# Kernel tuning notes

Measured on AMD Instinct MI355X. Metric: run time of the kernel, lower is better.

The kernel has to match this reference:

```python
import jax, jax.numpy as jnp
import numpy as np

H = 2048
D = 128            # align_dim
TEMP_TAU = 1.0
BIAS_MAX = 0.5
LN_EPS = 1e-5


def _ln(x, g, b):
    m = jnp.mean(x, axis=-1, keepdims=True)
    v = jnp.mean((x - m) ** 2, axis=-1, keepdims=True)
    return (x - m) / jnp.sqrt(v + LN_EPS) * g + b


def _mlp(x, g, b, W1, b1, W2, b2):
    # LayerNorm -> Linear -> GELU(exact) -> Linear
    h = jax.nn.gelu(_ln(x, g, b) @ W1.T + b1, approximate=False)
    return h @ W2.T + b2


def _l2n(x):
    n = jnp.linalg.norm(x, axis=-1, keepdims=True)
    return x / jnp.maximum(n, 1e-12)


def setup_inputs() -> dict:
    key = jax.random.key(0)
    ks = jax.random.split(key, 20)
    B, L = 4096, 4096
    d2 = 2 * D
    s_h = 1.0 / np.sqrt(H)
    s_d2 = 1.0 / np.sqrt(d2)
    inp = {
        "q": jax.random.normal(ks[0], (B, H), jnp.float32),
        "R_non": jax.random.normal(ks[1], (L, H), jnp.float32),
        # mlp_q
        "ln_q_g": jnp.ones((H,), jnp.float32),
        "ln_q_b": jnp.zeros((H,), jnp.float32),
        "W1q": jax.random.uniform(ks[2], (d2, H), jnp.float32, -s_h, s_h),
        "b1q": jnp.zeros((d2,), jnp.float32),
        "W2q": jax.random.uniform(ks[3], (D, d2), jnp.float32, -s_d2, s_d2),
        "b2q": jnp.zeros((D,), jnp.float32),
        # mlp_r
        "ln_r_g": jnp.ones((H,), jnp.float32),
        "ln_r_b": jnp.zeros((H,), jnp.float32),
        "W1r": jax.random.uniform(ks[4], (d2, H), jnp.float32, -s_h, s_h),
        "b1r": jnp.zeros((d2,), jnp.float32),
        "W2r": jax.random.uniform(ks[5], (D, d2), jnp.float32, -s_d2, s_d2),
        "b2r": jnp.zeros((D,), jnp.float32),
        # mlp_dec (input 2D=256 -> 128 -> 1)
        "ln_d_g": jnp.ones((d2,), jnp.float32),
        "ln_d_b": jnp.zeros((d2,), jnp.float32),
        "W1d": jax.random.uniform(ks[6], (128, d2), jnp.float32, -s_d2, s_d2),
        "b1d": jnp.zeros((128,), jnp.float32),
        "W2d": jax.random.uniform(ks[7], (1, 128), jnp.float32, -1 / np.sqrt(128), 1 / np.sqrt(128)),
        "b2d": jnp.zeros((1,), jnp.float32),
        # scalar heads
        "beta": jax.random.uniform(ks[8], (2,), jnp.float32, -0.1, 0.1),
        "W_len": jax.random.uniform(ks[9], (1, 2), jnp.float32, -0.1, 0.1),
        "b_len": jnp.zeros((1,), jnp.float32),
    }
    return inp


def reference(q, R_non, ln_q_g, ln_q_b, W1q, b1q, W2q, b2q,
              ln_r_g, ln_r_b, W1r, b1r, W2r, b2r,
              ln_d_g, ln_d_b, W1d, b1d, W2d, b2d,
              beta, W_len, b_len):
    L = R_non.shape[0]
    z_q = _l2n(_mlp(q, ln_q_g, ln_q_b, W1q, b1q, W2q, b2q))          # [B, D]
    Z_r = _l2n(_mlp(R_non, ln_r_g, ln_r_b, W1r, b1r, W2r, b2r))      # [L, D]
    scores = (z_q @ Z_r.T) / jnp.sqrt(jnp.float32(D))                 # [B, L]
    attn = jax.nn.softmax(scores, axis=-1)                            # [B, L]
    r_bar = _l2n(attn @ Z_r)                                          # [B, D]
    inter = jnp.concatenate([z_q, r_bar], axis=-1)                    # [B, 2D]
    raw_logit = _mlp(inter, ln_d_g, ln_d_b, W1d, b1d, W2d, b2d)[..., 0]  # [B]
    cos_q_r = jnp.sum(z_q * r_bar, axis=-1)                           # [B]
    entropy = -jnp.sum(attn * jnp.log(attn + 1e-8), axis=-1)          # [B]
    u_n = entropy / jnp.log(jnp.float32(L))                           # [B]
    sf = jnp.stack([cos_q_r, u_n], axis=-1)                           # [B, 2]
    delta_len_norm = (sf @ W_len.T + b_len)[..., 0]                   # [B]
    len_feat = jnp.tanh(delta_len_norm / TEMP_TAU)
    delta_theta = jnp.clip(beta[0] * u_n + beta[1] * len_feat, -BIAS_MAX, BIAS_MAX)
    return raw_logit, delta_theta
```

## Files before the change

### kernel.cpp

```cpp
#include <hip/hip_runtime.h>
#include <math.h>


#define HD   2048
#define D2   256
#define DD   128
#define NQ   4096
#define NT   8192
#define NSPLIT 16
#define KPS  (NQ / NSPLIT)
#define NIT  (KPS / 64)

typedef __attribute__((ext_vector_type(8))) short s16x8;
typedef __attribute__((ext_vector_type(4))) float f32x4;

static __device__ __forceinline__ float gelu_exact(float x){
    return 0.5f * x * (1.0f + erff(x * 0.7071067811865475f));
}
static __device__ __forceinline__ unsigned short f2bf(float f){
    unsigned int u = __float_as_uint(f);
    return (unsigned short)((u + 0x7FFFu + ((u >> 16) & 1u)) >> 16);
}
static __device__ __forceinline__ unsigned int pack2bf(float a, float b){
    return (unsigned int)f2bf(a) | ((unsigned int)f2bf(b) << 16);
}

static __device__ __forceinline__ void gload_lds16(const void* g, void* l){
    __builtin_amdgcn_global_load_lds(
        (const __attribute__((address_space(1))) unsigned int*)g,
        (__attribute__((address_space(3))) unsigned int*)l, 16, 0, 0);
}

__global__ __launch_bounds__(256)
void kLN_cast(const float* __restrict__ q, const float* __restrict__ R,
              const float* __restrict__ gq, const float* __restrict__ bq,
              const float* __restrict__ gr, const float* __restrict__ br,
              const float* __restrict__ W1q, const float* __restrict__ W1r,
              unsigned short* __restrict__ Xbf, unsigned short* __restrict__ Wbf){
    const int r = blockIdx.x;
    const int tid = threadIdx.x;
    if (r >= NT){
        const int rw = r - NT;
        const float* src = (rw >= 256) ? (W1r + (size_t)(rw - 256) * HD)
                                       : (W1q + (size_t)rw * HD);
        float4 a = *(const float4*)&src[tid * 8];
        float4 c = *(const float4*)&src[tid * 8 + 4];
        uint4 p = {pack2bf(a.x, a.y), pack2bf(a.z, a.w),
                   pack2bf(c.x, c.y), pack2bf(c.z, c.w)};
        *(uint4*)&Wbf[(size_t)rw * HD + tid * 8] = p;
        return;
    }
    const float* src = (r < NQ) ? (q + (size_t)r * HD) : (R + (size_t)(r - NQ) * HD);
    const float* g  = (r < NQ) ? gq : gr;
    const float* bb = (r < NQ) ? bq : br;
    float4 x0 = *(const float4*)&src[tid * 8];
    float4 x1 = *(const float4*)&src[tid * 8 + 4];
    float v[8] = {x0.x, x0.y, x0.z, x0.w, x1.x, x1.y, x1.z, x1.w};
    float s = 0.f, sq = 0.f;
#pragma unroll
    for (int i = 0; i < 8; ++i){ s += v[i]; sq += v[i] * v[i]; }
#pragma unroll
    for (int off = 32; off > 0; off >>= 1){
        s  += __shfl_xor(s, off);
        sq += __shfl_xor(sq, off);
    }
    __shared__ float wS[4], wQ[4];
    const int wave = tid >> 6, lane = tid & 63;
    if (lane == 0){ wS[wave] = s; wQ[wave] = sq; }
    __syncthreads();
    float sum = wS[0] + wS[1] + wS[2] + wS[3];
    float sqs = wQ[0] + wQ[1] + wQ[2] + wQ[3];
    float mean = sum * (1.0f / HD);
    float var  = sqs * (1.0f / HD) - mean * mean;
    float rstd = rsqrtf(fmaxf(var, 0.0f) + 1e-5f);
    float4 g0 = *(const float4*)&g[tid * 8];
    float4 g1 = *(const float4*)&g[tid * 8 + 4];
    float4 b0 = *(const float4*)&bb[tid * 8];
    float4 b1 = *(const float4*)&bb[tid * 8 + 4];
    float gg[8] = {g0.x, g0.y, g0.z, g0.w, g1.x, g1.y, g1.z, g1.w};
    float bv[8] = {b0.x, b0.y, b0.z, b0.w, b1.x, b1.y, b1.z, b1.w};
    float h[8];
#pragma unroll
    for (int i = 0; i < 8; ++i) h[i] = (v[i] - mean) * rstd * gg[i] + bv[i];
    uint4 p = {pack2bf(h[0], h[1]), pack2bf(h[2], h[3]),
               pack2bf(h[4], h[5]), pack2bf(h[6], h[7])};
    *(uint4*)&Xbf[(size_t)r * HD + tid * 8] = p;
}

__global__ __launch_bounds__(256)
void k2_mfma(const unsigned short* __restrict__ Xbf,
             const unsigned short* __restrict__ Wbf,
             float* __restrict__ HP){
    const int tid  = threadIdx.x;
    const int wave = tid >> 6, lane = tid & 63;
    const int quad = lane >> 4, col = lane & 15;
    const int mblk = blockIdx.x;
    const int nblk = blockIdx.y;
    const int ks   = blockIdx.z;
    const int inp  = mblk >> 6;
    const int mbase = mblk * 64;
    const int nbase = nblk * 128;
    const int wm = wave & 1, wn = wave >> 1;

    __shared__ __align__(16) char smem[49152];

    const unsigned short* gA[2];
    const unsigned short* gB[4];
#pragma unroll
    for (int i = 0; i < 2; ++i){
        int s = i * 256 + wave * 64 + lane;
        int row = s >> 3, c = (s & 7) ^ (row & 7);
        gA[i] = Xbf + (size_t)(mbase + row) * HD + ks * 1024 + c * 8;
    }
#pragma unroll
    for (int j = 0; j < 4; ++j){
        int s = j * 256 + wave * 64 + lane;
        int row = s >> 3, c = (s & 7) ^ (row & 7);
        gB[j] = Wbf + (size_t)(inp * 256 + nbase + row) * HD + ks * 1024 + c * 8;
    }

#define K2_STAGE(d, k0)                                                        \
    {                                                                          \
        _Pragma("unroll")                                                      \
        for (int i = 0; i < 2; ++i)                                            \
            gload_lds16(gA[i] + (k0),                                          \
                        smem + (d) * 24576 + (i * 256 + wave * 64 + lane) * 16);\
        _Pragma("unroll")                                                      \
        for (int j = 0; j < 4; ++j)                                            \
            gload_lds16(gB[j] + (k0),                                          \
                        smem + (d) * 24576 + 8192 + (j * 256 + wave * 64 + lane) * 16);\
    }

    int aoff[2][2], boff[4][2];
#pragma unroll
    for (int mi = 0; mi < 2; ++mi){
        int ra = wm * 32 + mi * 16 + col;
#pragma unroll
        for (int kst = 0; kst < 2; ++kst){
            int cc = kst * 4 + quad;
            aoff[mi][kst] = ra * 128 + ((cc ^ (ra & 7)) << 4);
        }
    }
#pragma unroll
    for (int ni = 0; ni < 4; ++ni){
        int rb = wn * 64 + ni * 16 + col;
#pragma unroll
        for (int kst = 0; kst < 2; ++kst){
            int cc = kst * 4 + quad;
            boff[ni][kst] = rb * 128 + ((cc ^ (rb & 7)) << 4);
        }
    }

    f32x4 acc[2][4];
#pragma unroll
    for (int mi = 0; mi < 2; ++mi)
#pragma unroll
        for (int ni = 0; ni < 4; ++ni) acc[mi][ni] = (f32x4){0.f, 0.f, 0.f, 0.f};

    int cur = 0;
    K2_STAGE(0, 0);
    __syncthreads();
    for (int t = 0; t < 16; ++t){
        if (t < 15) K2_STAGE(cur ^ 1, (t + 1) * 64);
        const char* Ab = smem + cur * 24576;
        const char* Bb = Ab + 8192;
        s16x8 a[2][2], b[4][2];
#pragma unroll
        for (int mi = 0; mi < 2; ++mi)
#pragma unroll
            for (int kst = 0; kst < 2; ++kst)
                a[mi][kst] = *(const s16x8*)(Ab + aoff[mi][kst]);
#pragma unroll
        for (int ni = 0; ni < 4; ++ni)
#pragma unroll
            for (int kst = 0; kst < 2; ++kst)
                b[ni][kst] = *(const s16x8*)(Bb + boff[ni][kst]);
#pragma unroll
        for (int kst = 0; kst < 2; ++kst)
#pragma unroll
            for (int mi = 0; mi < 2; ++mi)
#pragma unroll
                for (int ni = 0; ni < 4; ++ni)
                    acc[mi][ni] = __builtin_amdgcn_mfma_f32_16x16x32_bf16(
                        a[mi][kst], b[ni][kst], acc[mi][ni], 0, 0, 0);
        __syncthreads();
        cur ^= 1;
    }
#undef K2_STAGE

    float* dst = HP + (size_t)ks * NT * D2;
#pragma unroll
    for (int mi = 0; mi < 2; ++mi){
#pragma unroll
        for (int ni = 0; ni < 4; ++ni){
#pragma unroll
            for (int reg = 0; reg < 4; ++reg){
                int m = mbase + wm * 32 + mi * 16 + quad * 4 + reg;
                int n = nbase + wn * 64 + ni * 16 + col;
                dst[(size_t)m * D2 + n] = acc[mi][ni][reg];
            }
        }
    }
}

__global__ __launch_bounds__(256)
void k3_gemm2(const float* __restrict__ HP,
              const float* __restrict__ b1q, const float* __restrict__ b1r,
              const float* __restrict__ W2q, const float* __restrict__ b2q,
              const float* __restrict__ W2r, const float* __restrict__ b2r,
              float* __restrict__ Z, unsigned short* __restrict__ Zbf){
    const int gstart = blockIdx.x * 16;
    const int inp = (gstart >= NQ) ? 1 : 0;
    const float* b1 = inp ? b1r : b1q;
    const float* W2 = inp ? W2r : W2q;
    const float* b2 = inp ? b2r : b2q;

    __shared__ __align__(16) float Hs[16][68];
    __shared__ __align__(16) float Wk[64][132];
    __shared__ float red[16][17];
    __shared__ float normS[16];

    const int tid = threadIdx.x;
    const int ty = tid >> 4;
    const int tx = tid & 15;

    float acc[8];
#pragma unroll
    for (int jj = 0; jj < 8; ++jj) acc[jj] = 0.f;

    for (int kc = 0; kc < 4; ++kc){
#pragma unroll
        for (int i = 0; i < 4; ++i){
            int e = tid + i * 256;
            int rr = e >> 6, kk = e & 63;
            size_t idx = (size_t)(gstart + rr) * D2 + kc * 64 + kk;
            float hv = HP[idx] + HP[(size_t)NT * D2 + idx] + b1[kc * 64 + kk];
            Hs[rr][kk] = gelu_exact(hv);
        }
#pragma unroll
        for (int i = 0; i < 32; ++i){
            int e = tid + i * 256;
            int nn = e >> 6, kk = e & 63;
            Wk[kk][nn] = W2[(size_t)nn * D2 + kc * 64 + kk];
        }
        __syncthreads();
#pragma unroll
        for (int k4 = 0; k4 < 16; ++k4){
            float a0[4];
            float4 t0 = *(const float4*)&Hs[ty][k4 * 4];
            a0[0] = t0.x; a0[1] = t0.y; a0[2] = t0.z; a0[3] = t0.w;
#pragma unroll
            for (int kq = 0; kq < 4; ++kq){
                float4 w0 = *(const float4*)&Wk[k4 * 4 + kq][tx * 8];
                float4 w1 = *(const float4*)&Wk[k4 * 4 + kq][tx * 8 + 4];
                float wv[8] = {w0.x, w0.y, w0.z, w0.w, w1.x, w1.y, w1.z, w1.w};
#pragma unroll
                for (int jj = 0; jj < 8; ++jj)
                    acc[jj] += a0[kq] * wv[jj];
            }
        }
        __syncthreads();
    }
    float v0[8];
    float sq0 = 0.f;
#pragma unroll
    for (int jj = 0; jj < 8; ++jj){
        int c = tx * 8 + jj;
        v0[jj] = acc[jj] + b2[c];
        sq0 += v0[jj] * v0[jj];
    }
    red[ty][tx] = sq0;
    __syncthreads();
    if (tid < 16){
        float s = 0.f;
#pragma unroll
        for (int t = 0; t < 16; ++t) s += red[tid][t];
        normS[tid] = 1.0f / fmaxf(sqrtf(s), 1e-12f);
    }
    __syncthreads();
    float s0 = normS[ty];
    int row0 = gstart + ty;
    size_t o0 = (size_t)row0 * DD + tx * 8;
    float z0[8];
#pragma unroll
    for (int jj = 0; jj < 8; ++jj) z0[jj] = v0[jj] * s0;
    float4 a = {z0[0], z0[1], z0[2], z0[3]}, b = {z0[4], z0[5], z0[6], z0[7]};
    *(float4*)&Z[o0]     = a;  *(float4*)&Z[o0 + 4] = b;
    uint4 p0 = {pack2bf(z0[0], z0[1]), pack2bf(z0[2], z0[3]),
                pack2bf(z0[4], z0[5]), pack2bf(z0[6], z0[7])};
    *(uint4*)&Zbf[o0] = p0;
}

__global__ __launch_bounds__(256)
void kT_transpose(const unsigned short* __restrict__ Zbf,
                  unsigned short* __restrict__ ZbfT){
    __shared__ unsigned short Ts[64][129];
    const int r0 = blockIdx.x * 64;
    const int tid = threadIdx.x;
#pragma unroll
    for (int i = 0; i < 32; ++i){
        int e = tid + i * 256;
        int rr = e >> 7, dd = e & 127;
        Ts[rr][dd] = Zbf[(size_t)(NQ + r0 + rr) * DD + dd];
    }
    __syncthreads();
#pragma unroll
    for (int i = 0; i < 32; ++i){
        int e = tid + i * 256;
        int dd = e >> 6, rr = e & 63;
        ZbfT[(size_t)dd * NQ + r0 + rr] = Ts[rr][dd];
    }
}

__global__ __launch_bounds__(256)
void kA_attn(const unsigned short* __restrict__ Zbf,
             const unsigned short* __restrict__ ZbfT,
             float* __restrict__ OP, float* __restrict__ LW){
    const int tid  = threadIdx.x;
    const int wave = tid >> 6, lane = tid & 63;
    const int quad = lane >> 4, col = lane & 15;
    const int m0   = blockIdx.x * 128 + wave * 32;
    const int split = blockIdx.y;
    const float scl = 0.08838834764831845f;

    __shared__ __align__(16) char sK[16384];
    __shared__ __align__(16) char sV[16384];
    __shared__ __align__(16) unsigned short Pt[4][2][16][72];

    s16x8 aq[2][4];
#pragma unroll
    for (int m = 0; m < 2; ++m)
#pragma unroll
        for (int kb = 0; kb < 4; ++kb)
            aq[m][kb] = *(const s16x8*)&Zbf[(size_t)(m0 + m * 16 + col) * DD + kb * 32 + quad * 8];

    const unsigned short* gK[4];
    const unsigned short* gV[4];
    int dK[4], dV[4];
#pragma unroll
    for (int i = 0; i < 4; ++i){
        int s = i * 256 + tid;
        int row = s >> 4, c = (s & 15) ^ (row & 15);
        gK[i] = Zbf + (size_t)(NQ + row) * DD + c * 8;
        dK[i] = s * 16;
        int s2 = i * 256 + tid;
        int rv = s2 >> 3, cv = (s2 & 7) ^ (rv & 7);
        gV[i] = ZbfT + (size_t)rv * NQ + cv * 8;
        dV[i] = s2 * 16;
    }

    int kOff[4][4];
#pragma unroll
    for (int nt = 0; nt < 4; ++nt){
        int rb = nt * 16 + col;
#pragma unroll
        for (int kb = 0; kb < 4; ++kb)
            kOff[nt][kb] = rb * 256 + (((kb * 4 + quad) ^ (rb & 15)) << 4);
    }
    int vOff[8][2];
#pragma unroll
    for (int dt = 0; dt < 8; ++dt){
        int rv = dt * 16 + col;
#pragma unroll
        for (int kb2 = 0; kb2 < 2; ++kb2)
            vOff[dt][kb2] = rv * 128 + (((kb2 * 4 + quad) ^ (rv & 7)) << 4);
    }

    f32x4 o[2][8];
#pragma unroll
    for (int m = 0; m < 2; ++m)
#pragma unroll
        for (int dt = 0; dt < 8; ++dt) o[m][dt] = (f32x4){0.f, 0.f, 0.f, 0.f};
    float lp[2][4] = {{0.f,0.f,0.f,0.f},{0.f,0.f,0.f,0.f}};
    float wp[2][4] = {{0.f,0.f,0.f,0.f},{0.f,0.f,0.f,0.f}};

    for (int it = 0; it < NIT; ++it){
        const int r0 = split * KPS + it * 64;
#pragma unroll
        for (int i = 0; i < 4; ++i)
            gload_lds16(gK[i] + (size_t)r0 * DD, sK + dK[i]);
#pragma unroll
        for (int i = 0; i < 4; ++i)
            gload_lds16(gV[i] + r0, sV + dV[i]);
        __syncthreads();

#pragma unroll
        for (int nt = 0; nt < 4; ++nt){
            s16x8 b[4];
#pragma unroll
            for (int kb = 0; kb < 4; ++kb)
                b[kb] = *(const s16x8*)(sK + kOff[nt][kb]);
#pragma unroll
            for (int m = 0; m < 2; ++m){
                f32x4 s = (f32x4){0.f, 0.f, 0.f, 0.f};
#pragma unroll
                for (int kb = 0; kb < 4; ++kb)
                    s = __builtin_amdgcn_mfma_f32_16x16x32_bf16(aq[m][kb], b[kb], s, 0, 0, 0);
#pragma unroll
                for (int reg = 0; reg < 4; ++reg){
                    float sv = s[reg] * scl;
                    float e  = __expf(sv);
                    lp[m][reg] += e;
                    wp[m][reg] += e * sv;
                    Pt[wave][m][quad * 4 + reg][nt * 16 + col] = f2bf(e);
                }
            }
        }

        s16x8 ap[2][2];
#pragma unroll
        for (int m = 0; m < 2; ++m)
#pragma unroll
            for (int kb2 = 0; kb2 < 2; ++kb2)
                ap[m][kb2] = *(const s16x8*)&Pt[wave][m][col][kb2 * 32 + quad * 8];
#pragma unroll
        for (int dt = 0; dt < 8; ++dt){
#pragma unroll
            for (int kb2 = 0; kb2 < 2; ++kb2){
                s16x8 b = *(const s16x8*)(sV + vOff[dt][kb2]);
                o[0][dt] = __builtin_amdgcn_mfma_f32_16x16x32_bf16(ap[0][kb2], b, o[0][dt], 0, 0, 0);
                o[1][dt] = __builtin_amdgcn_mfma_f32_16x16x32_bf16(ap[1][kb2], b, o[1][dt], 0, 0, 0);
            }
        }
        __syncthreads();
    }

#pragma unroll
    for (int m = 0; m < 2; ++m)
#pragma unroll
    for (int reg = 0; reg < 4; ++reg){
        float l = lp[m][reg], w = wp[m][reg];
        l += __shfl_xor(l, 8);  w += __shfl_xor(w, 8);
        l += __shfl_xor(l, 4);  w += __shfl_xor(w, 4);
        l += __shfl_xor(l, 2);  w += __shfl_xor(w, 2);
        l += __shfl_xor(l, 1);  w += __shfl_xor(w, 1);
        if (col == 0){
            int row = m0 + m * 16 + quad * 4 + reg;
            LW[((size_t)row * NSPLIT + split) * 2]     = l;
            LW[((size_t)row * NSPLIT + split) * 2 + 1] = w;
        }
    }
#pragma unroll
    for (int m = 0; m < 2; ++m)
#pragma unroll
    for (int dt = 0; dt < 8; ++dt){
#pragma unroll
        for (int reg = 0; reg < 4; ++reg){
            int row = m0 + m * 16 + quad * 4 + reg;
            OP[((size_t)row * NSPLIT + split) * DD + dt * 16 + col] = o[m][dt][reg];
        }
    }
}

__global__ __launch_bounds__(256)
void k8_decoder(const float* __restrict__ Z, const float* __restrict__ OP,
                const float* __restrict__ LW,
                const float* __restrict__ gd, const float* __restrict__ bd,
                const float* __restrict__ W1d, const float* __restrict__ b1d,
                const float* __restrict__ W2d, const float* __restrict__ b2d,
                const float* __restrict__ beta, const float* __restrict__ W_len,
                const float* __restrict__ b_len,
                float* __restrict__ out){
    const int r0 = blockIdx.x * 4;
    const int tid = threadIdx.x;
    const int wave = tid >> 6, lane = tid & 63;
    const int row = r0 + wave;

    __shared__ __align__(16) float Xs[4][256];
    __shared__ __align__(16) float Wd[128][33];
    __shared__ float RBs[4][128];
    __shared__ float pr[4][2];
    __shared__ float cosS[4], uS[4];

    {
        const int c0 = lane * 2;
        float v0 = 0.f, v1 = 0.f;
#pragma unroll
        for (int s = 0; s < NSPLIT; ++s){
            float2 t = *(const float2*)&OP[((size_t)row * NSPLIT + s) * DD + c0];
            v0 += t.x; v1 += t.y;
        }
        float ss = v0 * v0 + v1 * v1;
#pragma unroll
        for (int off = 32; off > 0; off >>= 1) ss += __shfl_xor(ss, off);
        float scale = 1.0f / fmaxf(sqrtf(ss), 1e-12f);
        float rb0 = v0 * scale, rb1 = v1 * scale;
        RBs[wave][c0]     = rb0;
        RBs[wave][c0 + 1] = rb1;
        float2 zq = *(const float2*)&Z[(size_t)row * DD + c0];
        float cz = zq.x * rb0 + zq.y * rb1;
#pragma unroll
        for (int off = 32; off > 0; off >>= 1) cz += __shfl_xor(cz, off);
        float l_p = 0.f, w_p = 0.f;
        if (lane < NSPLIT){
            float2 lw = *(const float2*)&LW[((size_t)row * NSPLIT + lane) * 2];
            l_p = lw.x; w_p = lw.y;
        }
#pragma unroll
        for (int off = 8; off > 0; off >>= 1){
            l_p += __shfl_xor(l_p, off);
            w_p += __shfl_xor(w_p, off);
        }
        if (lane == 0){
            cosS[wave] = cz;
            float ent = logf(l_p) - w_p / l_p;
            uS[wave] = ent * (1.0f / 8.317766166719343f);
        }
    }
    __syncthreads();

    {
        const int c0 = lane * 4;
        float4 v;
        if (c0 < DD) v = *(const float4*)&Z[(size_t)row * DD + c0];
        else         v = *(const float4*)&RBs[wave][c0 - DD];
        float s  = v.x + v.y + v.z + v.w;
        float sq = v.x * v.x + v.y * v.y + v.z * v.z + v.w * v.w;
#pragma unroll
        for (int off = 32; off > 0; off >>= 1){
            s  += __shfl_xor(s, off);
            sq += __shfl_xor(sq, off);
        }
        float mean = s * (1.0f / D2);
        float var  = sq * (1.0f / D2) - mean * mean;
        float rstd = rsqrtf(fmaxf(var, 0.0f) + 1e-5f);
        float4 g = *(const float4*)&gd[c0];
        float4 b = *(const float4*)&bd[c0];
        float4 xn;
        xn.x = (v.x - mean) * rstd * g.x + b.x;
        xn.y = (v.y - mean) * rstd * g.y + b.y;
        xn.z = (v.z - mean) * rstd * g.z + b.z;
        xn.w = (v.w - mean) * rstd * g.w + b.w;
        *(float4*)&Xs[wave][c0] = xn;
    }
    __syncthreads();

    const int j  = tid & 127;
    const int rp = tid >> 7;
    const float* xa = &Xs[rp * 2][0];
    const float* xb = &Xs[rp * 2 + 1][0];
    float h0 = 0.f, h1 = 0.f;
    for (int cch = 0; cch < 8; ++cch){
#pragma unroll
        for (int i = 0; i < 16; ++i){
            int e = tid + i * 256;
            int j2 = e >> 5, kk = e & 31;
            Wd[j2][kk] = W1d[(size_t)j2 * D2 + cch * 32 + kk];
        }
        __syncthreads();
#pragma unroll
        for (int k4 = 0; k4 < 8; ++k4){
            float4 w  = *(const float4*)&Wd[j][k4 * 4];
            float4 a4 = *(const float4*)&xa[cch * 32 + k4 * 4];
            float4 b4 = *(const float4*)&xb[cch * 32 + k4 * 4];
            h0 += w.x * a4.x + w.y * a4.y + w.z * a4.z + w.w * a4.w;
            h1 += w.x * b4.x + w.y * b4.y + w.z * b4.z + w.w * b4.w;
        }
        __syncthreads();
    }
    float bj = b1d[j];
    h0 = gelu_exact(h0 + bj);
    h1 = gelu_exact(h1 + bj);
    float w2 = W2d[j];
    float p0 = h0 * w2, p1 = h1 * w2;
#pragma unroll
    for (int off = 32; off > 0; off >>= 1){
        p0 += __shfl_xor(p0, off);
        p1 += __shfl_xor(p1, off);
    }
    if (lane == 0){ pr[wave][0] = p0; pr[wave][1] = p1; }
    __syncthreads();

    if (tid < 4){
        const int rw    = tid;
        const int rpair = rw >> 1, rlo = rw & 1;
        float lg = b2d[0] + pr[rpair * 2][rlo] + pr[rpair * 2 + 1][rlo];
        const int gr = r0 + rw;
        float u  = uS[rw];
        float cv = cosS[rw];
        float dln = cv * W_len[0] + u * W_len[1] + b_len[0];
        float dt = beta[0] * u + beta[1] * tanhf(dln);
        dt = fminf(0.5f, fmaxf(-0.5f, dt));
        out[gr]      = lg;
        out[NQ + gr] = dt;
    }
}

extern "C" void kernel_launch(void* const* d_in, const int* in_sizes, int n_in,
                              void* d_out, int out_size, void* d_ws, size_t ws_size,
                              hipStream_t stream){
    const float* q      = (const float*)d_in[0];
    const float* R      = (const float*)d_in[1];
    const float* ln_q_g = (const float*)d_in[2];
    const float* ln_q_b = (const float*)d_in[3];
    const float* W1q    = (const float*)d_in[4];
    const float* b1q    = (const float*)d_in[5];
    const float* W2q    = (const float*)d_in[6];
    const float* b2q    = (const float*)d_in[7];
    const float* ln_r_g = (const float*)d_in[8];
    const float* ln_r_b = (const float*)d_in[9];
    const float* W1r    = (const float*)d_in[10];
    const float* b1r    = (const float*)d_in[11];
    const float* W2r    = (const float*)d_in[12];
    const float* b2r    = (const float*)d_in[13];
    const float* ln_d_g = (const float*)d_in[14];
    const float* ln_d_b = (const float*)d_in[15];
    const float* W1d    = (const float*)d_in[16];
    const float* b1d    = (const float*)d_in[17];
    const float* W2d    = (const float*)d_in[18];
    const float* b2d    = (const float*)d_in[19];
    const float* beta   = (const float*)d_in[20];
    const float* W_len  = (const float*)d_in[21];
    const float* b_len  = (const float*)d_in[22];

    float* WS = (float*)d_ws;
    unsigned short* Xbf  = (unsigned short*)(WS);
    float* OP    = WS;
    float* HP    = WS + 8388608;
    float* LW    = WS + 8388608;
    unsigned short* Wbf  = (unsigned short*)(WS + 12582912);
    float* Z     = WS + 13107200;
    unsigned short* Zbf  = (unsigned short*)(WS + 14155776);
    unsigned short* ZbfT = (unsigned short*)(WS + 14680064);
    float* out   = (float*)d_out;

    hipLaunchKernelGGL(kLN_cast, dim3(NT + 512), dim3(256), 0, stream,
                       q, R, ln_q_g, ln_q_b, ln_r_g, ln_r_b, W1q, W1r, Xbf, Wbf);
    hipLaunchKernelGGL(k2_mfma, dim3(128, 2, 2), dim3(256), 0, stream, Xbf, Wbf, HP);
    hipLaunchKernelGGL(k3_gemm2, dim3(512), dim3(256), 0, stream,
                       HP, b1q, b1r, W2q, b2q, W2r, b2r, Z, Zbf);
    hipLaunchKernelGGL(kT_transpose, dim3(64), dim3(256), 0, stream, Zbf, ZbfT);
    hipLaunchKernelGGL(kA_attn, dim3(32, NSPLIT), dim3(256), 0, stream, Zbf, ZbfT, OP, LW);
    hipLaunchKernelGGL(k8_decoder, dim3(1024), dim3(256), 0, stream,
                       Z, OP, LW, ln_d_g, ln_d_b, W1d, b1d, W2d, b2d,
                       beta, W_len, b_len, out);
}
```

Measured before the change: 242.5 us.

## Double-buffer K/V tiles in attention kernel and reorganize partial-output layout

The attention kernel now uses dynamic shared memory with two K/V stage buffers, so the async global-to-LDS loads for the next tile are issued before computing on the current one. A barrier per iteration is removed. The per-wave P tile is halved by processing the two 16-row groups one after the other, which reuses one Pt buffer. The split-partial outputs OP/LW are stored split-major instead of row-major, and the decoder reads them to match. Shared memory per block grows to about 73KB, which may cut occupancy. Pt reuse between the m-iterations within a wave depends on wave-local ordering and has no explicit sync.

```diff
diff --git a/kernel.cpp b/kernel.cpp
--- a/kernel.cpp
+++ b/kernel.cpp
@@ -316,6 +316,7 @@
 void kA_attn(const unsigned short* __restrict__ Zbf,
              const unsigned short* __restrict__ ZbfT,
              float* __restrict__ OP, float* __restrict__ LW){
+    extern __shared__ __align__(16) char smem[];
     const int tid  = threadIdx.x;
     const int wave = tid >> 6, lane = tid & 63;
     const int quad = lane >> 4, col = lane & 15;
@@ -323,9 +324,7 @@
     const int split = blockIdx.y;
     const float scl = 0.08838834764831845f;
 
-    __shared__ __align__(16) char sK[16384];
-    __shared__ __align__(16) char sV[16384];
-    __shared__ __align__(16) unsigned short Pt[4][2][16][72];
+    unsigned short (*Pt)[16][72] = (unsigned short(*)[16][72])(smem + 65536);
 
     s16x8 aq[2][4];
 #pragma unroll
@@ -349,6 +348,19 @@
         dV[i] = s2 * 16;
     }
 
+#define KA_STAGE(d, t)                                                         \
+    {                                                                          \
+        const int rr0 = split * KPS + (t) * 64;                                \
+        char* kb_ = smem + (d) * 16384;                                        \
+        char* vb_ = smem + 32768 + (d) * 16384;                                \
+        _Pragma("unroll")                                                      \
+        for (int i = 0; i < 4; ++i)                                            \
+            gload_lds16(gK[i] + (size_t)rr0 * DD, kb_ + dK[i]);                \
+        _Pragma("unroll")                                                      \
+        for (int i = 0; i < 4; ++i)                                            \
+            gload_lds16(gV[i] + rr0, vb_ + dV[i]);                             \
+    }
+
     int kOff[4][4];
 #pragma unroll
     for (int nt = 0; nt < 4; ++nt){
@@ -374,24 +386,22 @@
     float lp[2][4] = {{0.f,0.f,0.f,0.f},{0.f,0.f,0.f,0.f}};
     float wp[2][4] = {{0.f,0.f,0.f,0.f},{0.f,0.f,0.f,0.f}};
 
+    KA_STAGE(0, 0);
+    __syncthreads();
+    int cur = 0;
     for (int it = 0; it < NIT; ++it){
-        const int r0 = split * KPS + it * 64;
-#pragma unroll
-        for (int i = 0; i < 4; ++i)
-            gload_lds16(gK[i] + (size_t)r0 * DD, sK + dK[i]);
-#pragma unroll
-        for (int i = 0; i < 4; ++i)
-            gload_lds16(gV[i] + r0, sV + dV[i]);
-        __syncthreads();
-
-#pragma unroll
-        for (int nt = 0; nt < 4; ++nt){
-            s16x8 b[4];
-#pragma unroll
-            for (int kb = 0; kb < 4; ++kb)
-                b[kb] = *(const s16x8*)(sK + kOff[nt][kb]);
-#pragma unroll
-            for (int m = 0; m < 2; ++m){
+        if (it + 1 < NIT) KA_STAGE(cur ^ 1, it + 1);
+        const char* Kb = smem + cur * 16384;
+        const char* Vb = smem + 32768 + cur * 16384;
+
+#pragma unroll
+        for (int m = 0; m < 2; ++m){
+#pragma unroll
+            for (int nt = 0; nt < 4; ++nt){
+                s16x8 b[4];
+#pragma unroll
+                for (int kb = 0; kb < 4; ++kb)
+                    b[kb] = *(const s16x8*)(Kb + kOff[nt][kb]);
                 f32x4 s = (f32x4){0.f, 0.f, 0.f, 0.f};
 #pragma unroll
                 for (int kb = 0; kb < 4; ++kb)
@@ -402,28 +412,26 @@
                     float e  = __expf(sv);
                     lp[m][reg] += e;
                     wp[m][reg] += e * sv;
-                    Pt[wave][m][quad * 4 + reg][nt * 16 + col] = f2bf(e);
+                    Pt[wave][quad * 4 + reg][nt * 16 + col] = f2bf(e);
                 }
             }
-        }
-
-        s16x8 ap[2][2];
-#pragma unroll
-        for (int m = 0; m < 2; ++m)
+            s16x8 ap[2];
 #pragma unroll
             for (int kb2 = 0; kb2 < 2; ++kb2)
-                ap[m][kb2] = *(const s16x8*)&Pt[wave][m][col][kb2 * 32 + quad * 8];
-#pragma unroll
-        for (int dt = 0; dt < 8; ++dt){
-#pragma unroll
-            for (int kb2 = 0; kb2 < 2; ++kb2){
-                s16x8 b = *(const s16x8*)(sV + vOff[dt][kb2]);
-                o[0][dt] = __builtin_amdgcn_mfma_f32_16x16x32_bf16(ap[0][kb2], b, o[0][dt], 0, 0, 0);
-                o[1][dt] = __builtin_amdgcn_mfma_f32_16x16x32_bf16(ap[1][kb2], b, o[1][dt], 0, 0, 0);
+                ap[kb2] = *(const s16x8*)&Pt[wave][col][kb2 * 32 + quad * 8];
+#pragma unroll
+            for (int dt = 0; dt < 8; ++dt){
+#pragma unroll
+                for (int kb2 = 0; kb2 < 2; ++kb2){
+                    s16x8 b = *(const s16x8*)(Vb + vOff[dt][kb2]);
+                    o[m][dt] = __builtin_amdgcn_mfma_f32_16x16x32_bf16(ap[kb2], b, o[m][dt], 0, 0, 0);
+                }
             }
         }
         __syncthreads();
-    }
+        cur ^= 1;
+    }
+#undef KA_STAGE
 
 #pragma unroll
     for (int m = 0; m < 2; ++m)
@@ -436,8 +444,8 @@
         l += __shfl_xor(l, 1);  w += __shfl_xor(w, 1);
         if (col == 0){
             int row = m0 + m * 16 + quad * 4 + reg;
-            LW[((size_t)row * NSPLIT + split) * 2]     = l;
-            LW[((size_t)row * NSPLIT + split) * 2 + 1] = w;
+            LW[((size_t)split * NQ + row) * 2]     = l;
+            LW[((size_t)split * NQ + row) * 2 + 1] = w;
         }
     }
 #pragma unroll
@@ -447,7 +455,7 @@
 #pragma unroll
         for (int reg = 0; reg < 4; ++reg){
             int row = m0 + m * 16 + quad * 4 + reg;
-            OP[((size_t)row * NSPLIT + split) * DD + dt * 16 + col] = o[m][dt][reg];
+            OP[((size_t)split * NQ + row) * DD + dt * 16 + col] = o[m][dt][reg];
         }
     }
 }
@@ -477,7 +485,7 @@
         float v0 = 0.f, v1 = 0.f;
 #pragma unroll
         for (int s = 0; s < NSPLIT; ++s){
-            float2 t = *(const float2*)&OP[((size_t)row * NSPLIT + s) * DD + c0];
+            float2 t = *(const float2*)&OP[((size_t)s * NQ + row) * DD + c0];
             v0 += t.x; v1 += t.y;
         }
         float ss = v0 * v0 + v1 * v1;
@@ -493,7 +501,7 @@
         for (int off = 32; off > 0; off >>= 1) cz += __shfl_xor(cz, off);
         float l_p = 0.f, w_p = 0.f;
         if (lane < NSPLIT){
-            float2 lw = *(const float2*)&LW[((size_t)row * NSPLIT + lane) * 2];
+            float2 lw = *(const float2*)&LW[((size_t)lane * NQ + row) * 2];
             l_p = lw.x; w_p = lw.y;
         }
 #pragma unroll
@@ -630,7 +638,8 @@
     hipLaunchKernelGGL(k3_gemm2, dim3(512), dim3(256), 0, stream,
                        HP, b1q, b1r, W2q, b2q, W2r, b2r, Z, Zbf);
     hipLaunchKernelGGL(kT_transpose, dim3(64), dim3(256), 0, stream, Zbf, ZbfT);
-    hipLaunchKernelGGL(kA_attn, dim3(32, NSPLIT), dim3(256), 0, stream, Zbf, ZbfT, OP, LW);
+    hipLaunchKernelGGL(kA_attn, dim3(32, NSPLIT), dim3(256), 74752, stream,
+                       Zbf, ZbfT, OP, LW);
     hipLaunchKernelGGL(k8_decoder, dim3(1024), dim3(256), 0, stream,
                        Z, OP, LW, ln_d_g, ln_d_b, W1d, b1d, W2d, b2d,
                        beta, W_len, b_len, out);
```

New measurement: 236.6 us. 1.03x faster.
